# Kernel optimization log

Measured on AMD Instinct MI355X. Metric: run time of the kernel, lower is better.

## Reference

```python
import math
import jax, jax.numpy as jnp
from jax import lax
import numpy as np

D = 256; H = 8; NL = 6; HALF = D // 2
B = 32; NEV = 256

def sinpos(x):
    # SinusoidalPosEmb: (..., ) int -> (..., D)
    freq = jnp.exp(jnp.arange(HALF, dtype=jnp.float32) * (-math.log(10000.0) / (HALF - 1)))
    e = x.astype(jnp.float32)[..., None] * freq
    return jnp.concatenate([jnp.sin(e), jnp.cos(e)], axis=-1)

def layer_norm(x, g, b, eps=1e-5):
    m = x.mean(-1, keepdims=True)
    v = ((x - m) ** 2).mean(-1, keepdims=True)
    return (x - m) / jnp.sqrt(v + eps) * g + b

def gelu(x):
    return jax.nn.gelu(x, approximate=False)

def conv1d(x, w, b, stride):
    y = lax.conv_general_dilated(x, w, (stride,), [(3, 3)], dimension_numbers=("NCH", "OIH", "NCH"))
    return y + b[None, :, None]

def setup_inputs():
    ks = iter(jax.random.split(jax.random.key(0), 48))
    def p(*shape):
        return jax.random.normal(next(ks), shape, dtype=jnp.float32) * 0.02
    inp = dict(
        mel=jax.random.normal(next(ks), (B, 80, 2000), dtype=jnp.float32),
        events=jnp.sort(jax.random.randint(next(ks), (B, NEV), 0, 2000), axis=-1),
        event_mask=jnp.zeros((B, NEV), dtype=bool),
        star_rating=jax.random.uniform(next(ks), (B,), dtype=jnp.float32) * 9.0,
        mel_W=p(16, 80), mel_b=p(16),
        conv1_w=p(128, 16, 7), conv1_b=p(128),
        gn_g=jnp.ones(128, jnp.float32), gn_b=jnp.zeros(128, jnp.float32),
        conv2_w=p(256, 128, 7), conv2_b=p(256),
        cn_g=jnp.ones(D, jnp.float32), cn_b=jnp.zeros(D, jnp.float32),
        star_table=p(20, D),
        ep_W1=p(D, 3 * D), ep_b1=p(D), ep_W2=p(D, D), ep_b2=p(D),
        tl_Wqkv=p(NL, 3 * D, D), tl_bqkv=p(NL, 3 * D),
        tl_Wo=p(NL, D, D), tl_bo=p(NL, D),
        tl_ln1g=jnp.ones((NL, D), jnp.float32), tl_ln1b=jnp.zeros((NL, D), jnp.float32),
        tl_ln2g=jnp.ones((NL, D), jnp.float32), tl_ln2b=jnp.zeros((NL, D), jnp.float32),
        tl_W1=p(NL, 4 * D, D), tl_b1=p(NL, 4 * D),
        tl_W2=p(NL, D, 4 * D), tl_b2=p(NL, D),
        pool_q=jax.random.normal(next(ks), (D,), dtype=jnp.float32),
        on_g=jnp.ones(D, jnp.float32), on_b=jnp.zeros(D, jnp.float32),
        oh_W=p(1, D), oh_b=p(1),
    )
    return inp

def reference(mel, events, event_mask, star_rating, mel_W, mel_b, conv1_w, conv1_b, gn_g, gn_b, conv2_w, conv2_b, cn_g, cn_b, star_table, ep_W1, ep_b1, ep_W2, ep_b2, tl_Wqkv, tl_bqkv, tl_Wo, tl_bo, tl_ln1g, tl_ln1b, tl_ln2g, tl_ln2b, tl_W1, tl_b1, tl_W2, tl_b2, pool_q, on_g, on_b, oh_W, oh_b):
    Bsz = mel.shape[0]
    # mel_compress on channel dim: (B,80,T) -> (B,16,T)
    x_mel = jnp.einsum('bct,oc->bot', mel, mel_W) + mel_b[None, :, None]
    h = gelu(conv1d(x_mel, conv1_w, conv1_b, 2))           # (B,128,1000)
    # GroupNorm(1, C): normalize over (C, L) per sample
    m = h.mean((1, 2), keepdims=True)
    v = ((h - m) ** 2).mean((1, 2), keepdims=True)
    h = (h - m) / jnp.sqrt(v + 1e-5) * gn_g[None, :, None] + gn_b[None, :, None]
    h = gelu(conv1d(h, conv2_w, conv2_b, 2))               # (B,256,500)
    x = h.transpose(0, 2, 1)                               # (B,500,256)
    x = layer_norm(x, cn_g, cn_b)
    S = x.shape[1]
    x = x + sinpos(jnp.arange(S))[None]
    star_bucket = jnp.clip((star_rating / 0.5).astype(jnp.int32), 0, star_table.shape[0] - 1)
    x = x + star_table[star_bucket][:, None, :]
    # --- event gap/ratio embeddings (vectorized; exact match to torch loop when all valid) ---
    diff = jnp.maximum(events[:, 1:] - events[:, :-1], 1)  # clamp(min=1)
    g = jnp.concatenate([diff[:, :1], diff], axis=1)        # g[0] = g[1]
    gap_ms = g * 5
    g_f = jnp.maximum(g.astype(jnp.float32), 1.0)
    r = jnp.clip(g_f[:, 1:] / g_f[:, :-1], 0.1, 10.0)
    ones = jnp.ones((Bsz, 1), dtype=jnp.float32)
    ratio_before = (jnp.concatenate([ones, r], axis=1) * 50).astype(jnp.int32)
    ratio_after = (jnp.concatenate([r, ones], axis=1) * 50).astype(jnp.int32)
    combined = jnp.concatenate([sinpos(ratio_before), sinpos(ratio_after), sinpos(gap_ms)], axis=-1)
    ev = gelu(combined @ ep_W1.T + ep_b1) @ ep_W2.T + ep_b2
    ev = jnp.where(event_mask[..., None], 0.0, ev)
    token_pos = jnp.clip(events // 4, 0, S - 1)
    # batched scatter-add of event embeddings into token stream
    x = x.at[jnp.arange(Bsz)[:, None], token_pos].add(ev)
    hd = D // H
    for i in range(NL):
        xn = layer_norm(x, tl_ln1g[i], tl_ln1b[i])
        qkv = xn @ tl_Wqkv[i].T + tl_bqkv[i]
        q, k, vv = jnp.split(qkv, 3, axis=-1)
        q = q.reshape(Bsz, S, H, hd).transpose(0, 2, 1, 3)
        k = k.reshape(Bsz, S, H, hd).transpose(0, 2, 1, 3)
        vv = vv.reshape(Bsz, S, H, hd).transpose(0, 2, 1, 3)
        a = jax.nn.softmax(jnp.einsum('bhqd,bhkd->bhqk', q, k) / math.sqrt(hd), axis=-1)
        o = jnp.einsum('bhqk,bhkd->bhqd', a, vv).transpose(0, 2, 1, 3).reshape(Bsz, S, D)
        x = x + o @ tl_Wo[i].T + tl_bo[i]
        xn = layer_norm(x, tl_ln2g[i], tl_ln2b[i])
        x = x + gelu(xn @ tl_W1[i].T + tl_b1[i]) @ tl_W2[i].T + tl_b2[i]
    # attention pooling + head
    logits = x @ pool_q / math.sqrt(D)
    w = jax.nn.softmax(logits, axis=-1)
    pooled = jnp.einsum('bs,bsd->bd', w, x)
    return (layer_norm(pooled, on_g, on_b) @ oh_W.T + oh_b).squeeze(-1)
```

## Files before the change

### kernel.cpp

```cpp
#include <hip/hip_runtime.h>
#include <math.h>

namespace {
constexpr int kB = 32;
constexpr int kS = 500;
constexpr int kH = 8;
}
#define LKC (-0.07252236513366287)

typedef __attribute__((ext_vector_type(8))) short s16x8;
typedef __attribute__((ext_vector_type(4))) float f32x4;

__device__ __forceinline__ float gelu_f(float x){
  return 0.5f * x * (1.0f + erff(x * 0.7071067811865476f));
}
__device__ __forceinline__ float b2f(short s){
  union { unsigned u; float f; } x; x.u = ((unsigned)(unsigned short)s) << 16; return x.f;
}
__device__ __forceinline__ short f2b(float f){
  unsigned u = __float_as_uint(f);
  unsigned r = (u + 0x7fffu + ((u >> 16) & 1u)) >> 16;
  return (short)r;
}
__device__ __forceinline__ unsigned cvtpk(float lo, float hi){
  unsigned r;
  asm("v_cvt_pk_bf16_f32 %0, %1, %2" : "=v"(r) : "v"(lo), "v"(hi));
  return r;
}

__global__ __launch_bounds__(256) void f2b_kernel(const float* __restrict__ in,
    short* __restrict__ out, int n){
  int i = blockIdx.x * 256 + threadIdx.x;
  if(i < n) out[i] = f2b(in[i]);
}
__global__ __launch_bounds__(128) void conv1w_pad(const float* __restrict__ w, short* __restrict__ out){
  int n = blockIdx.x, k = threadIdx.x;
  out[n*128 + k] = (k < 112) ? f2b(w[n*112 + k]) : (short)0;
}

template<int OUT, bool DOGELU>
__global__ __launch_bounds__(256) void gemm_mfma(const short* __restrict__ A,
    const short* __restrict__ W, const float* __restrict__ bias,
    void* __restrict__ Cv, int M, int N, int K){
  __shared__ __align__(16) short Al[128*64];
  __shared__ __align__(16) short Wl[128*64];
  const int t = threadIdx.x;
  const int wid = t >> 6, lane = t & 63;
  const int m0 = blockIdx.y * 128, n0 = blockIdx.x * 128;
  const int wr = (wid >> 1) * 64, wc = (wid & 1) * 64;
  const int frow = lane & 15, lg = lane >> 4;
  const int rA = t >> 3;
  const int sA = (t & 7) ^ (rA & 7);
  const short* Aq = A + (size_t)(m0 + rA) * K + sA * 8;
  const short* Wq = W + (size_t)(n0 + rA) * K + sA * 8;
  f32x4 acc[4][4] = {};
  for(int k0 = 0; k0 < K; k0 += 64){
    s16x8 av[4], wv[4];
    #pragma unroll
    for(int j = 0; j < 4; ++j){
      av[j] = *(const s16x8*)(Aq + k0 + (size_t)(32*j)*K);
      wv[j] = *(const s16x8*)(Wq + k0 + (size_t)(32*j)*K);
    }
    __syncthreads();
    #pragma unroll
    for(int j = 0; j < 4; ++j){
      *(s16x8*)&Al[t*8 + j*2048] = av[j];
      *(s16x8*)&Wl[t*8 + j*2048] = wv[j];
    }
    __syncthreads();
    #pragma unroll
    for(int kh = 0; kh < 2; ++kh){
      s16x8 a[4], b[4];
      #pragma unroll
      for(int mi = 0; mi < 4; ++mi){
        int r = wr + mi*16 + frow;
        a[mi] = *(const s16x8*)&Al[r*64 + (((kh*4 + lg) ^ (r & 7)) * 8)];
      }
      #pragma unroll
      for(int ni = 0; ni < 4; ++ni){
        int r = wc + ni*16 + frow;
        b[ni] = *(const s16x8*)&Wl[r*64 + (((kh*4 + lg) ^ (r & 7)) * 8)];
      }
      #pragma unroll
      for(int mi = 0; mi < 4; ++mi)
        #pragma unroll
        for(int ni = 0; ni < 4; ++ni)
          acc[mi][ni] = __builtin_amdgcn_mfma_f32_16x16x32_bf16(a[mi], b[ni], acc[mi][ni], 0, 0, 0);
    }
  }
  #pragma unroll
  for(int mi = 0; mi < 4; ++mi){
    #pragma unroll
    for(int ni = 0; ni < 4; ++ni){
      const int col = n0 + wc + ni*16 + (lane & 15);
      const float bv = bias[col];
      #pragma unroll
      for(int r = 0; r < 4; ++r){
        const int row = m0 + wr + mi*16 + (lane >> 4)*4 + r;
        float v = acc[mi][ni][r] + bv;
        if(DOGELU) v = gelu_f(v);
        if(OUT == 0) ((float*)Cv)[(size_t)row*N + col] = v;
        else if(OUT == 1) ((float*)Cv)[(size_t)row*N + col] += v;
        else ((short*)Cv)[(size_t)row*N + col] = f2b(v);
      }
    }
  }
}

template<bool DOGELU>
__global__ __launch_bounds__(512) void gemm512(const short* __restrict__ A,
    const short* __restrict__ W, const float* __restrict__ bias,
    short* __restrict__ C, int M, int N, int K){
  __shared__ __align__(16) short Al[128*64];
  __shared__ __align__(16) short Wl[256*64];
  const int t = threadIdx.x;
  const int wid = t >> 6, lane = t & 63;
  const int m0 = blockIdx.y * 128, n0 = blockIdx.x * 256;
  const int wm = wid >> 2, wn = wid & 3;
  const int frow = lane & 15, lg = lane >> 4;
  const int rA = t >> 3;
  const int sA = (t & 7) ^ (rA & 7);
  const short* Aq = A + (size_t)(m0 + rA) * K + sA * 8;
  const short* Wq = W + (size_t)(n0 + rA) * K + sA * 8;
  f32x4 acc[4][4] = {};
  for(int k0 = 0; k0 < K; k0 += 64){
    s16x8 av[2], wv[4];
    av[0] = *(const s16x8*)(Aq + k0);
    av[1] = *(const s16x8*)(Aq + k0 + (size_t)64*K);
    #pragma unroll
    for(int j = 0; j < 4; ++j)
      wv[j] = *(const s16x8*)(Wq + k0 + (size_t)(64*j)*K);
    __syncthreads();
    *(s16x8*)&Al[t*8] = av[0];
    *(s16x8*)&Al[t*8 + 4096] = av[1];
    #pragma unroll
    for(int j = 0; j < 4; ++j)
      *(s16x8*)&Wl[t*8 + j*4096] = wv[j];
    __syncthreads();
    #pragma unroll
    for(int kh = 0; kh < 2; ++kh){
      s16x8 a[4], b[4];
      #pragma unroll
      for(int mi = 0; mi < 4; ++mi){
        int r = wm*64 + mi*16 + frow;
        a[mi] = *(const s16x8*)&Al[r*64 + (((kh*4 + lg) ^ (r & 7)) * 8)];
      }
      #pragma unroll
      for(int ni = 0; ni < 4; ++ni){
        int r = wn*64 + ni*16 + frow;
        b[ni] = *(const s16x8*)&Wl[r*64 + (((kh*4 + lg) ^ (r & 7)) * 8)];
      }
      #pragma unroll
      for(int mi = 0; mi < 4; ++mi)
        #pragma unroll
        for(int ni = 0; ni < 4; ++ni)
          acc[mi][ni] = __builtin_amdgcn_mfma_f32_16x16x32_bf16(a[mi], b[ni], acc[mi][ni], 0, 0, 0);
    }
  }
  #pragma unroll
  for(int mi = 0; mi < 4; ++mi){
    #pragma unroll
    for(int ni = 0; ni < 4; ++ni){
      const int col = n0 + wn*64 + ni*16 + (lane & 15);
      const float bv = bias[col];
      #pragma unroll
      for(int r = 0; r < 4; ++r){
        const int row = m0 + wm*64 + mi*16 + (lane >> 4)*4 + r;
        float v = acc[mi][ni][r] + bv;
        if(DOGELU) v = gelu_f(v);
        C[(size_t)row*N + col] = f2b(v);
      }
    }
  }
}

template<bool DOLN>
__global__ __launch_bounds__(512) void gemm_ln(const short* __restrict__ A,
    const short* __restrict__ W, const float* __restrict__ bias,
    float* __restrict__ X, const float* __restrict__ lg_, const float* __restrict__ lb_,
    short* __restrict__ XNB, int M, int K){
  __shared__ __align__(16) short Al[64*64];
  __shared__ __align__(16) short Wl[256*64];
  __shared__ float sbuf[64][4];
  const int t = threadIdx.x;
  const int wid = t >> 6, lane = t & 63;
  const int m0 = blockIdx.y * 64;
  const int wm = wid >> 2, wn = wid & 3;
  const int frow = lane & 15, lg = lane >> 4;
  const int lq = lane & 15;
  const int rA = t >> 3;
  const int sA = (t & 7) ^ (rA & 7);
  const short* Aq = A + (size_t)(m0 + rA) * K + sA * 8;
  const short* Wq = W + (size_t)rA * K + sA * 8;
  f32x4 acc[2][4] = {};
  for(int k0 = 0; k0 < K; k0 += 64){
    s16x8 av = *(const s16x8*)(Aq + k0);
    s16x8 wv[4];
    #pragma unroll
    for(int j = 0; j < 4; ++j)
      wv[j] = *(const s16x8*)(Wq + k0 + (size_t)(64*j)*K);
    __syncthreads();
    *(s16x8*)&Al[t*8] = av;
    #pragma unroll
    for(int j = 0; j < 4; ++j)
      *(s16x8*)&Wl[t*8 + j*4096] = wv[j];
    __syncthreads();
    #pragma unroll
    for(int kh = 0; kh < 2; ++kh){
      s16x8 a[2], b[4];
      #pragma unroll
      for(int mi = 0; mi < 2; ++mi){
        int r = wm*32 + mi*16 + frow;
        a[mi] = *(const s16x8*)&Al[r*64 + (((kh*4 + lg) ^ (r & 7)) * 8)];
      }
      #pragma unroll
      for(int ni = 0; ni < 4; ++ni){
        int r = wn*64 + ni*16 + frow;
        b[ni] = *(const s16x8*)&Wl[r*64 + (((kh*4 + lg) ^ (r & 7)) * 8)];
      }
      #pragma unroll
      for(int mi = 0; mi < 2; ++mi)
        #pragma unroll
        for(int ni = 0; ni < 4; ++ni)
          acc[mi][ni] = __builtin_amdgcn_mfma_f32_16x16x32_bf16(a[mi], b[ni], acc[mi][ni], 0, 0, 0);
    }
  }
  float v[2][4][4];
  #pragma unroll
  for(int mi = 0; mi < 2; ++mi)
    #pragma unroll
    for(int ni = 0; ni < 4; ++ni){
      const int col = wn*64 + ni*16 + lq;
      const float bv = bias[col];
      #pragma unroll
      for(int r = 0; r < 4; ++r){
        const int row = m0 + wm*32 + mi*16 + lg*4 + r;
        v[mi][ni][r] = acc[mi][ni][r] + bv + X[(size_t)row*256 + col];
      }
    }
  __syncthreads();
  float vmean[2][4], vrstd[2][4];
  if(DOLN){
    #pragma unroll
    for(int mi = 0; mi < 2; ++mi)
      #pragma unroll
      for(int r = 0; r < 4; ++r){
        float s = v[mi][0][r] + v[mi][1][r] + v[mi][2][r] + v[mi][3][r];
        s += __shfl_xor(s, 1); s += __shfl_xor(s, 2);
        s += __shfl_xor(s, 4); s += __shfl_xor(s, 8);
        if(lq == 0) sbuf[wm*32 + mi*16 + lg*4 + r][wn] = s;
      }
    __syncthreads();
    #pragma unroll
    for(int mi = 0; mi < 2; ++mi)
      #pragma unroll
      for(int r = 0; r < 4; ++r){
        int rl = wm*32 + mi*16 + lg*4 + r;
        vmean[mi][r] = (sbuf[rl][0] + sbuf[rl][1] + sbuf[rl][2] + sbuf[rl][3]) * (1.f/256.f);
      }
    __syncthreads();
    #pragma unroll
    for(int mi = 0; mi < 2; ++mi)
      #pragma unroll
      for(int r = 0; r < 4; ++r){
        float q = 0.f;
        #pragma unroll
        for(int ni = 0; ni < 4; ++ni){ float d = v[mi][ni][r] - vmean[mi][r]; q += d*d; }
        q += __shfl_xor(q, 1); q += __shfl_xor(q, 2);
        q += __shfl_xor(q, 4); q += __shfl_xor(q, 8);
        if(lq == 0) sbuf[wm*32 + mi*16 + lg*4 + r][wn] = q;
      }
    __syncthreads();
    #pragma unroll
    for(int mi = 0; mi < 2; ++mi)
      #pragma unroll
      for(int r = 0; r < 4; ++r){
        int rl = wm*32 + mi*16 + lg*4 + r;
        float Q = sbuf[rl][0] + sbuf[rl][1] + sbuf[rl][2] + sbuf[rl][3];
        vrstd[mi][r] = 1.f / sqrtf(Q * (1.f/256.f) + 1e-5f);
      }
  }
  #pragma unroll
  for(int mi = 0; mi < 2; ++mi)
    #pragma unroll
    for(int ni = 0; ni < 4; ++ni){
      const int col = wn*64 + ni*16 + lq;
      float gg = 0.f, bb = 0.f;
      if(DOLN){ gg = lg_[col]; bb = lb_[col]; }
      #pragma unroll
      for(int r = 0; r < 4; ++r){
        const int row = m0 + wm*32 + mi*16 + lg*4 + r;
        float val = v[mi][ni][r];
        X[(size_t)row*256 + col] = val;
        if(DOLN)
          XNB[(size_t)row*256 + col] = f2b((val - vmean[mi][r]) * vrstd[mi][r] * gg + bb);
      }
    }
}

__global__ __launch_bounds__(256) void mel_kernel(const float* __restrict__ mel,
    const float* __restrict__ W, const float* __restrict__ bias, float* __restrict__ xm){
  __shared__ float Ws[16][80];
  __shared__ float bs[16];
  const int t = threadIdx.x;
  for(int i = t; i < 16*80; i += 256) Ws[i/80][i%80] = W[i];
  if(t < 16) bs[t] = bias[t];
  __syncthreads();
  int blk = blockIdx.x;
  int b = blk >> 3;
  int tc = (blk & 7) * 256 + t;
  if(tc >= 2000) return;
  float acc[16];
  #pragma unroll
  for(int o = 0; o < 16; ++o) acc[o] = bs[o];
  for(int c = 0; c < 80; ++c){
    float v = mel[((size_t)b*80 + c)*2000 + tc];
    #pragma unroll
    for(int o = 0; o < 16; ++o) acc[o] += v * Ws[o][c];
  }
  #pragma unroll
  for(int o = 0; o < 16; ++o) xm[((size_t)b*16 + o)*2000 + tc] = acc[o];
}

__global__ __launch_bounds__(256) void im2col1b(const float* __restrict__ xm, short* __restrict__ A){
  size_t idx = (size_t)blockIdx.x * 256 + threadIdx.x;
  int col = idx & 127;
  size_t row = idx >> 7;
  int t1 = row % 1000, b = row / 1000;
  float v = 0.f;
  if(col < 112){
    int i = col / 7, k = col % 7;
    int src = 2*t1 + k - 3;
    if(src >= 0 && src < 2000) v = xm[((size_t)b*16 + i)*2000 + src];
  }
  A[idx] = f2b(v);
}

__global__ __launch_bounds__(256) void gn_part(const float* __restrict__ h1, double* __restrict__ part){
  int blk = blockIdx.x;
  const float* p = h1 + (size_t)blk * 16000;
  int t = threadIdx.x;
  double s = 0, q = 0;
  for(int i = t; i < 16000; i += 256){ double v = p[i]; s += v; q += v*v; }
  __shared__ double rs[256], rq[256];
  rs[t] = s; rq[t] = q; __syncthreads();
  for(int s2 = 128; s2 > 0; s2 >>= 1){
    if(t < s2){ rs[t] += rs[t+s2]; rq[t] += rq[t+s2]; }
    __syncthreads();
  }
  if(t == 0){ part[blk*2] = rs[0]; part[blk*2+1] = rq[0]; }
}
__global__ __launch_bounds__(256) void gn_final(const double* __restrict__ part, float* __restrict__ stats){
  int t = threadIdx.x;
  int b = t >> 3;
  double s = part[t*2], q = part[t*2+1];
  s += __shfl_xor(s, 1); q += __shfl_xor(q, 1);
  s += __shfl_xor(s, 2); q += __shfl_xor(q, 2);
  s += __shfl_xor(s, 4); q += __shfl_xor(q, 4);
  if((t & 7) == 0){
    double mean = s / 128000.0;
    double var  = q / 128000.0 - mean*mean;
    stats[b*2]   = (float)mean;
    stats[b*2+1] = (float)(1.0 / sqrt(var + 1e-5));
  }
}

__global__ __launch_bounds__(256) void im2col2b(const float* __restrict__ h1,
    const float* __restrict__ stats, const float* __restrict__ gg,
    const float* __restrict__ gb, short* __restrict__ A){
  size_t idx = (size_t)blockIdx.x * 256 + threadIdx.x;
  int col = idx % 896;
  size_t row = idx / 896;
  int t2 = row % 500, b = row / 500;
  int i = col / 7, k = col % 7;
  int src = 2*t2 + k - 3;
  float v = 0.f;
  if(src >= 0 && src < 1000){
    float raw = h1[((size_t)b*1000 + src)*128 + i];
    v = (raw - stats[b*2]) * stats[b*2+1] * gg[i] + gb[i];
  }
  A[idx] = f2b(v);
}

__global__ __launch_bounds__(256) void postconv(const float* __restrict__ xp,
    const float* __restrict__ cg, const float* __restrict__ cb,
    const float* __restrict__ star, const float* __restrict__ stab,
    float* __restrict__ x){
  int row = blockIdx.x, t = threadIdx.x;
  int s = row % 500, b = row / 500;
  __shared__ float red[256];
  float v = xp[(size_t)row*256 + t];
  red[t] = v; __syncthreads();
  for(int s2 = 128; s2 > 0; s2 >>= 1){ if(t < s2) red[t] += red[t+s2]; __syncthreads(); }
  float mean = red[0] / 256.f; __syncthreads();
  float d = v - mean;
  red[t] = d*d; __syncthreads();
  for(int s2 = 128; s2 > 0; s2 >>= 1){ if(t < s2) red[t] += red[t+s2]; __syncthreads(); }
  float rstd = 1.f / sqrtf(red[0]/256.f + 1e-5f);
  int j = t & 127;
  double f = exp((double)j * LKC);
  double a = (double)s * f;
  float pe = (float)(t < 128 ? sin(a) : cos(a));
  int bucket = (int)(star[b] * 2.0f);
  bucket = bucket < 0 ? 0 : (bucket > 19 ? 19 : bucket);
  x[(size_t)row*256 + t] = d*rstd*cg[t] + cb[t] + pe + stab[bucket*256 + t];
}

__global__ __launch_bounds__(256) void event_feat(const int* __restrict__ events, short* __restrict__ comb){
  int blk = blockIdx.x;
  int e = blk & 255, b = blk >> 8;
  const int* ev = events + b*256;
  int t = threadIdx.x;
  auto gof = [&](int i){ int j = i < 1 ? 1 : i; int d = ev[j] - ev[j-1]; return d < 1 ? 1 : d; };
  int gi = gof(e);
  double rb = 1.0, ra = 1.0;
  if(e != 0){
    rb = (double)gi / (double)gof(e-1);
    rb = rb < 0.1 ? 0.1 : (rb > 10.0 ? 10.0 : rb);
  }
  if(e != 255){
    ra = (double)gof(e+1) / (double)gi;
    ra = ra < 0.1 ? 0.1 : (ra > 10.0 ? 10.0 : ra);
  }
  int rbi = (int)(rb * 50.0);
  int rai = (int)(ra * 50.0);
  int gap = 5 * gi;
  int j = t & 127;
  double f = exp((double)j * LKC);
  double a0 = (double)rbi * f, a1 = (double)rai * f, a2 = (double)gap * f;
  size_t base = (size_t)blk * 768;
  comb[base + t]       = f2b((float)(t < 128 ? sin(a0) : cos(a0)));
  comb[base + 256 + t] = f2b((float)(t < 128 ? sin(a1) : cos(a1)));
  comb[base + 512 + t] = f2b((float)(t < 128 ? sin(a2) : cos(a2)));
}

__global__ __launch_bounds__(256) void ev_scatter(const float* __restrict__ evout,
    const int* __restrict__ events, const unsigned char* __restrict__ mask,
    float* __restrict__ x){
  int blk = blockIdx.x;
  int e = blk & 255, b = blk >> 8;
  if(mask[b*256 + e]) return;
  int tp = events[b*256 + e] >> 2;
  tp = tp < 0 ? 0 : (tp > 499 ? 499 : tp);
  int t = threadIdx.x;
  atomicAdd(&x[((size_t)b*500 + tp)*256 + t], evout[(size_t)blk*256 + t]);
}

__global__ __launch_bounds__(256) void ln_rows(const float* __restrict__ x,
    const float* __restrict__ g, const float* __restrict__ b, short* __restrict__ out){
  int row = blockIdx.x, t = threadIdx.x;
  int wid = t >> 6, lane = t & 63;
  __shared__ float sm[8];
  float v = x[(size_t)row*256 + t];
  float s = v;
  #pragma unroll
  for(int o = 1; o < 64; o <<= 1) s += __shfl_xor(s, o);
  if(lane == 0) sm[wid] = s;
  __syncthreads();
  float mean = (sm[0] + sm[1] + sm[2] + sm[3]) * (1.f/256.f);
  float d = v - mean;
  float q = d*d;
  #pragma unroll
  for(int o = 1; o < 64; o <<= 1) q += __shfl_xor(q, o);
  if(lane == 0) sm[4 + wid] = q;
  __syncthreads();
  float rstd = 1.f / sqrtf((sm[4] + sm[5] + sm[6] + sm[7]) * (1.f/256.f) + 1e-5f);
  out[(size_t)row*256 + t] = f2b(d*rstd*g[t] + b[t]);
}

__global__ __launch_bounds__(512) void attn_mfma(const short* __restrict__ qkv,
    short* __restrict__ o){
  __shared__ __align__(16) short Kl[512*40];
  __shared__ __align__(16) short Vt[32*520];
  __shared__ __align__(16) short Pl[8][640];
  const int i = blockIdx.x;
  const int b = (i & 7)*4 + ((i >> 3) & 3);
  const int h = i >> 5;
  const int t = threadIdx.x;
  const int wid = t >> 6, lane = t & 63;
  const int lq = lane & 15, lg = lane >> 4;
  const short* base = qkv + (size_t)b * kS * 768;
  {
    const int c = t & 3;
    for(int idx = t; idx < 2048; idx += 512){
      int row = idx >> 2;
      s16x8 kv = {0,0,0,0,0,0,0,0};
      unsigned vu0 = 0, vu1 = 0, vu2 = 0, vu3 = 0;
      if(row < kS){
        const short* rp = base + (size_t)row*768 + 256 + h*32 + c*8;
        kv = *(const s16x8*)rp;
        uint4 vv = *(const uint4*)(rp + 256);
        vu0 = vv.x; vu1 = vv.y; vu2 = vv.z; vu3 = vv.w;
      }
      *(s16x8*)&Kl[row*40 + c*8] = kv;
      unsigned b0 = (c & 2) ? vu2 : vu0, b1 = (c & 2) ? vu3 : vu1;
      unsigned b2 = (c & 2) ? vu0 : vu2, b3 = (c & 2) ? vu1 : vu3;
      unsigned r0 = (c & 1) ? b1 : b0, r1 = (c & 1) ? b2 : b1;
      unsigned r2 = (c & 1) ? b3 : b2, r3 = (c & 1) ? b0 : b3;
      #pragma unroll
      for(int j0 = 0; j0 < 8; ++j0){
        unsigned w = (j0 >> 1) == 0 ? r0 : (j0 >> 1) == 1 ? r1 : (j0 >> 1) == 2 ? r2 : r3;
        short val = (short)((j0 & 1) ? (w >> 16) : (w & 0xffff));
        int d = c*8 + ((j0 + 2*c) & 7);
        Vt[d*520 + row] = val;
      }
    }
  }
  __syncthreads();
  const float c2 = 0.17677669529663687f * 1.4426950408889634f;
  short* pw = &Pl[wid][0];
  for(int qi = 0; qi < 4; ++qi){
    const int qt = wid*4 + qi;
    const int q0 = qt*16;
    int qrow = q0 + lq; if(qrow > kS-1) qrow = kS-1;
    s16x8 qf = *(const s16x8*)(base + (size_t)qrow*768 + h*32 + lg*8);
    f32x4 sc[32];
    __builtin_amdgcn_s_setprio(1);
    #pragma unroll
    for(int kt = 0; kt < 32; ++kt){
      s16x8 kf = *(const s16x8*)&Kl[(kt*16 + lq)*40 + lg*8];
      f32x4 z = {0.f,0.f,0.f,0.f};
      sc[kt] = __builtin_amdgcn_mfma_f32_16x16x32_bf16(kf, qf, z, 0, 0, 0);
    }
    __builtin_amdgcn_s_setprio(0);
    if(lg >= 1){ sc[31][0] = -1e30f; sc[31][1] = -1e30f; sc[31][2] = -1e30f; sc[31][3] = -1e30f; }
    float l0 = 0.f, l1 = 0.f, l2 = 0.f, l3 = 0.f;
    #pragma unroll
    for(int kt = 0; kt < 32; ++kt){
      float p0 = exp2f(sc[kt][0] * c2);
      float p1 = exp2f(sc[kt][1] * c2);
      float p2 = exp2f(sc[kt][2] * c2);
      float p3 = exp2f(sc[kt][3] * c2);
      sc[kt][0] = p0; sc[kt][1] = p1; sc[kt][2] = p2; sc[kt][3] = p3;
      l0 += p0; l1 += p1; l2 += p2; l3 += p3;
    }
    float l = (l0 + l1) + (l2 + l3);
    l += __shfl_xor(l, 16, 64);
    l += __shfl_xor(l, 32, 64);
    f32x4 oa0 = {0.f,0.f,0.f,0.f}, oa1 = {0.f,0.f,0.f,0.f};
    #pragma unroll
    for(int kt2 = 0; kt2 < 16; ++kt2){
      f32x4 p0 = sc[kt2*2], p1 = sc[kt2*2+1];
      uint2 pk0, pk1;
      pk0.x = cvtpk(p0[0], p0[1]); pk0.y = cvtpk(p0[2], p0[3]);
      pk1.x = cvtpk(p1[0], p1[1]); pk1.y = cvtpk(p1[2], p1[3]);
      *(uint2*)&pw[lq*40 + lg*4] = pk0;
      *(uint2*)&pw[lq*40 + 16 + lg*4] = pk1;
      s16x8 pf = *(const s16x8*)&pw[lq*40 + lg*8];
      s16x8 v0 = *(const s16x8*)&Vt[lq*520 + kt2*32 + lg*8];
      s16x8 v1 = *(const s16x8*)&Vt[(16+lq)*520 + kt2*32 + lg*8];
      __builtin_amdgcn_s_setprio(1);
      oa0 = __builtin_amdgcn_mfma_f32_16x16x32_bf16(v0, pf, oa0, 0, 0, 0);
      oa1 = __builtin_amdgcn_mfma_f32_16x16x32_bf16(v1, pf, oa1, 0, 0, 0);
      __builtin_amdgcn_s_setprio(0);
    }
    float inv = 1.f / l;
    int qw = q0 + lq;
    if(qw < kS){
      short* op = o + ((size_t)(b*kS + qw))*256 + h*32;
      uint2 w0, w1;
      w0.x = cvtpk(oa0[0]*inv, oa0[1]*inv); w0.y = cvtpk(oa0[2]*inv, oa0[3]*inv);
      w1.x = cvtpk(oa1[0]*inv, oa1[1]*inv); w1.y = cvtpk(oa1[2]*inv, oa1[3]*inv);
      *(uint2*)&op[lg*4] = w0;
      *(uint2*)&op[16 + lg*4] = w1;
    }
  }
}

__global__ __launch_bounds__(256) void pool_head(const float* __restrict__ x,
    const float* __restrict__ pq, const float* __restrict__ og, const float* __restrict__ ob,
    const float* __restrict__ ohW, const float* __restrict__ ohb, float* __restrict__ out){
  int b = blockIdx.x, t = threadIdx.x;
  __shared__ float lg[500];
  __shared__ float red[256];
  const float* xb = x + (size_t)b * 500 * 256;
  for(int s = t; s < 500; s += 256){
    const float* xr = xb + (size_t)s * 256;
    float d = 0.f;
    for(int c = 0; c < 256; ++c) d += xr[c] * pq[c];
    lg[s] = d * 0.0625f;
  }
  __syncthreads();
  float m = -1e30f;
  for(int s = t; s < 500; s += 256) m = fmaxf(m, lg[s]);
  red[t] = m; __syncthreads();
  for(int s2 = 128; s2 > 0; s2 >>= 1){ if(t < s2) red[t] = fmaxf(red[t], red[t+s2]); __syncthreads(); }
  m = red[0]; __syncthreads();
  float ps = 0.f;
  for(int s = t; s < 500; s += 256){ float e = expf(lg[s] - m); lg[s] = e; ps += e; }
  red[t] = ps; __syncthreads();
  for(int s2 = 128; s2 > 0; s2 >>= 1){ if(t < s2) red[t] += red[t+s2]; __syncthreads(); }
  float inv = 1.f / red[0];
  __syncthreads();
  float acc = 0.f;
  for(int s = 0; s < 500; ++s) acc += lg[s] * xb[(size_t)s*256 + t];
  acc *= inv;
  __syncthreads();
  red[t] = acc; __syncthreads();
  for(int s2 = 128; s2 > 0; s2 >>= 1){ if(t < s2) red[t] += red[t+s2]; __syncthreads(); }
  float mean = red[0] / 256.f; __syncthreads();
  float d = acc - mean;
  red[t] = d*d; __syncthreads();
  for(int s2 = 128; s2 > 0; s2 >>= 1){ if(t < s2) red[t] += red[t+s2]; __syncthreads(); }
  float rstd = 1.f / sqrtf(red[0]/256.f + 1e-5f);
  __syncthreads();
  float val = (d*rstd*og[t] + ob[t]) * ohW[t];
  red[t] = val; __syncthreads();
  for(int s2 = 128; s2 > 0; s2 >>= 1){ if(t < s2) red[t] += red[t+s2]; __syncthreads(); }
  if(t == 0) out[b] = red[0] + ohb[0];
}

extern "C" void kernel_launch(void* const* d_in, const int* in_sizes, int n_in,
                              void* d_out, int out_size, void* d_ws, size_t ws_size,
                              hipStream_t stream){
  const float* mel      = (const float*)d_in[0];
  const int*   events   = (const int*)d_in[1];
  const unsigned char* emask = (const unsigned char*)d_in[2];
  const float* star     = (const float*)d_in[3];
  const float* mel_W    = (const float*)d_in[4];
  const float* mel_b    = (const float*)d_in[5];
  const float* conv1_w  = (const float*)d_in[6];
  const float* conv1_b  = (const float*)d_in[7];
  const float* gn_g     = (const float*)d_in[8];
  const float* gn_b     = (const float*)d_in[9];
  const float* conv2_w  = (const float*)d_in[10];
  const float* conv2_b  = (const float*)d_in[11];
  const float* cn_g     = (const float*)d_in[12];
  const float* cn_b     = (const float*)d_in[13];
  const float* star_tab = (const float*)d_in[14];
  const float* ep_W1    = (const float*)d_in[15];
  const float* ep_b1    = (const float*)d_in[16];
  const float* ep_W2    = (const float*)d_in[17];
  const float* ep_b2    = (const float*)d_in[18];
  const float* tl_Wqkv  = (const float*)d_in[19];
  const float* tl_bqkv  = (const float*)d_in[20];
  const float* tl_Wo    = (const float*)d_in[21];
  const float* tl_bo    = (const float*)d_in[22];
  const float* tl_ln1g  = (const float*)d_in[23];
  const float* tl_ln1b  = (const float*)d_in[24];
  const float* tl_ln2g  = (const float*)d_in[25];
  const float* tl_ln2b  = (const float*)d_in[26];
  const float* tl_W1    = (const float*)d_in[27];
  const float* tl_b1    = (const float*)d_in[28];
  const float* tl_W2    = (const float*)d_in[29];
  const float* tl_b2    = (const float*)d_in[30];
  const float* pool_q   = (const float*)d_in[31];
  const float* on_g     = (const float*)d_in[32];
  const float* on_b     = (const float*)d_in[33];
  const float* oh_W     = (const float*)d_in[34];
  const float* oh_b     = (const float*)d_in[35];
  (void)in_sizes; (void)n_in; (void)out_size; (void)ws_size;

  float* ws  = (float*)d_ws;
  float* X   = ws;
  short* XNB = (short*)(ws + 4096000);
  short* OB  = (short*)(ws + 6144000);
  short* WB  = (short*)(ws + 8192000);
  float* BIG = ws + 10812000;
  double* PART = (double*)(ws + 28668000);
  float* STATS = ws + 28671900;

  short* WBc1 = WB + 0;
  short* WBc2 = WB + 16384;
  short* WBe1 = WB + 245760;
  short* WBe2 = WB + 442368;
  short* WBqk = WB + 507904;
  short* WBwo = WB + 1687552;
  short* WBw1 = WB + 2080768;
  short* WBw2 = WB + 3653632;

  float* XMEL = BIG;
  short* A1B  = (short*)(BIG + 1024000);
  float* H1   = BIG + 3072000;
  short* A2B  = (short*)(BIG + 7168000);
  float* XPRE = BIG;
  short* COMBB= (short*)BIG;
  short* EHIDB= (short*)(BIG + 3146000);
  float* EVO  = BIG + 4195000;
  short* QKVB = (short*)BIG;
  short* HIDB = (short*)(BIG + 7168000);

  conv1w_pad<<<128, 128, 0, stream>>>(conv1_w, WBc1);
  f2b_kernel<<<896, 256, 0, stream>>>(conv2_w, WBc2, 229376);
  f2b_kernel<<<768, 256, 0, stream>>>(ep_W1, WBe1, 196608);
  f2b_kernel<<<256, 256, 0, stream>>>(ep_W2, WBe2, 65536);
  f2b_kernel<<<4608, 256, 0, stream>>>(tl_Wqkv, WBqk, 1179648);
  f2b_kernel<<<1536, 256, 0, stream>>>(tl_Wo, WBwo, 393216);
  f2b_kernel<<<6144, 256, 0, stream>>>(tl_W1, WBw1, 1572864);
  f2b_kernel<<<6144, 256, 0, stream>>>(tl_W2, WBw2, 1572864);

  mel_kernel<<<kB*8, 256, 0, stream>>>(mel, mel_W, mel_b, XMEL);
  im2col1b<<<16000, 256, 0, stream>>>(XMEL, A1B);
  gemm_mfma<0,true><<<dim3(1, 250), 256, 0, stream>>>(A1B, WBc1, conv1_b, H1, 32000, 128, 128);
  gn_part<<<256, 256, 0, stream>>>(H1, PART);
  gn_final<<<1, 256, 0, stream>>>(PART, STATS);
  im2col2b<<<56000, 256, 0, stream>>>(H1, STATS, gn_g, gn_b, A2B);
  gemm_mfma<0,true><<<dim3(2, 125), 256, 0, stream>>>(A2B, WBc2, conv2_b, XPRE, 16000, 256, 896);
  postconv<<<16000, 256, 0, stream>>>(XPRE, cn_g, cn_b, star, star_tab, X);
  event_feat<<<kB*256, 256, 0, stream>>>(events, COMBB);
  gemm_mfma<2,true><<<dim3(2, 64), 256, 0, stream>>>(COMBB, WBe1, ep_b1, EHIDB, 8192, 256, 768);
  gemm_mfma<0,false><<<dim3(2, 64), 256, 0, stream>>>(EHIDB, WBe2, ep_b2, EVO, 8192, 256, 256);
  ev_scatter<<<kB*256, 256, 0, stream>>>(EVO, events, emask, X);

  ln_rows<<<16000, 256, 0, stream>>>(X, tl_ln1g, tl_ln1b, XNB);
  for(int i = 0; i < 6; ++i){
    gemm512<false><<<dim3(3, 125), 512, 0, stream>>>(XNB, WBqk + (size_t)i*196608, tl_bqkv + i*768, QKVB, 16000, 768, 256);
    attn_mfma<<<kB*kH, 512, 0, stream>>>(QKVB, OB);
    gemm_ln<true><<<dim3(1, 250), 512, 0, stream>>>(OB, WBwo + (size_t)i*65536, tl_bo + i*256,
        X, tl_ln2g + i*256, tl_ln2b + i*256, XNB, 16000, 256);
    gemm512<true><<<dim3(4, 125), 512, 0, stream>>>(XNB, WBw1 + (size_t)i*262144, tl_b1 + i*1024, HIDB, 16000, 1024, 256);
    if(i < 5)
      gemm_ln<true><<<dim3(1, 250), 512, 0, stream>>>(HIDB, WBw2 + (size_t)i*262144, tl_b2 + i*256,
          X, tl_ln1g + (i+1)*256, tl_ln1b + (i+1)*256, XNB, 16000, 1024);
    else
      gemm_ln<false><<<dim3(1, 250), 512, 0, stream>>>(HIDB, WBw2 + (size_t)i*262144, tl_b2 + i*256,
          X, tl_ln1g, tl_ln1b, XNB, 16000, 1024);
  }

  pool_head<<<kB, 256, 0, stream>>>(X, pool_q, on_g, on_b, oh_W, oh_b, (float*)d_out);
}
```

Measured before the change: 870.8 us.

## Split attention blocks by query half, shuffle P fragments, fuse weight conversions

The attention kernel now launches twice as many blocks, each handling half of the query tiles for a (batch, head) pair. This raises occupancy across the CUs, at the cost of loading K and V into LDS twice. The P-matrix repack through a per-wave LDS scratch is replaced by cross-lane shuffles, which removes the LDS store and load round trip. The seven separate fp32-to-bf16 weight conversion launches are merged into one kernel to cut launch overhead.

```diff
diff --git a/kernel.cpp b/kernel.cpp
--- a/kernel.cpp
+++ b/kernel.cpp
@@ -28,14 +28,26 @@
   return r;
 }
 
-__global__ __launch_bounds__(256) void f2b_kernel(const float* __restrict__ in,
-    short* __restrict__ out, int n){
-  int i = blockIdx.x * 256 + threadIdx.x;
-  if(i < n) out[i] = f2b(in[i]);
-}
 __global__ __launch_bounds__(128) void conv1w_pad(const float* __restrict__ w, short* __restrict__ out){
   int n = blockIdx.x, k = threadIdx.x;
   out[n*128 + k] = (k < 112) ? f2b(w[n*112 + k]) : (short)0;
+}
+
+__global__ __launch_bounds__(256) void f2b_all(const float* __restrict__ c2,
+    const float* __restrict__ e1, const float* __restrict__ e2,
+    const float* __restrict__ qk, const float* __restrict__ wo,
+    const float* __restrict__ w1, const float* __restrict__ w2,
+    short* __restrict__ WB){
+  int blk = blockIdx.x, t = threadIdx.x;
+  const float* src; short* dst; int idx;
+  if(blk < 896){        src = c2; dst = WB + 16384;   idx = blk*256 + t; }
+  else if(blk < 1664){  src = e1; dst = WB + 245760;  idx = (blk-896)*256 + t; }
+  else if(blk < 1920){  src = e2; dst = WB + 442368;  idx = (blk-1664)*256 + t; }
+  else if(blk < 6528){  src = qk; dst = WB + 507904;  idx = (blk-1920)*256 + t; }
+  else if(blk < 8064){  src = wo; dst = WB + 1687552; idx = (blk-6528)*256 + t; }
+  else if(blk < 14208){ src = w1; dst = WB + 2080768; idx = (blk-8064)*256 + t; }
+  else {                src = w2; dst = WB + 3653632; idx = (blk-14208)*256 + t; }
+  dst[idx] = f2b(src[idx]);
 }
 
 template<int OUT, bool DOGELU>
@@ -472,10 +484,10 @@
     short* __restrict__ o){
   __shared__ __align__(16) short Kl[512*40];
   __shared__ __align__(16) short Vt[32*520];
-  __shared__ __align__(16) short Pl[8][640];
   const int i = blockIdx.x;
   const int b = (i & 7)*4 + ((i >> 3) & 3);
-  const int h = i >> 5;
+  const int h = (i >> 5) & 7;
+  const int half = i >> 8;
   const int t = threadIdx.x;
   const int wid = t >> 6, lane = t & 63;
   const int lq = lane & 15, lg = lane >> 4;
@@ -508,9 +520,8 @@
   }
   __syncthreads();
   const float c2 = 0.17677669529663687f * 1.4426950408889634f;
-  short* pw = &Pl[wid][0];
-  for(int qi = 0; qi < 4; ++qi){
-    const int qt = wid*4 + qi;
+  for(int qi = 0; qi < 2; ++qi){
+    const int qt = half*16 + wid*2 + qi;
     const int q0 = qt*16;
     int qrow = q0 + lq; if(qrow > kS-1) qrow = kS-1;
     s16x8 qf = *(const s16x8*)(base + (size_t)qrow*768 + h*32 + lg*8);
@@ -537,16 +548,27 @@
     float l = (l0 + l1) + (l2 + l3);
     l += __shfl_xor(l, 16, 64);
     l += __shfl_xor(l, 32, 64);
+    const int s0l = lq + ((lg & 1) << 5);
+    const int s1l = s0l + 16;
+    const bool fh = (lg & 2) != 0;
     f32x4 oa0 = {0.f,0.f,0.f,0.f}, oa1 = {0.f,0.f,0.f,0.f};
     #pragma unroll
     for(int kt2 = 0; kt2 < 16; ++kt2){
       f32x4 p0 = sc[kt2*2], p1 = sc[kt2*2+1];
-      uint2 pk0, pk1;
-      pk0.x = cvtpk(p0[0], p0[1]); pk0.y = cvtpk(p0[2], p0[3]);
-      pk1.x = cvtpk(p1[0], p1[1]); pk1.y = cvtpk(p1[2], p1[3]);
-      *(uint2*)&pw[lq*40 + lg*4] = pk0;
-      *(uint2*)&pw[lq*40 + 16 + lg*4] = pk1;
-      s16x8 pf = *(const s16x8*)&pw[lq*40 + lg*8];
+      unsigned pk00 = cvtpk(p0[0], p0[1]);
+      unsigned pk01 = cvtpk(p0[2], p0[3]);
+      unsigned pk10 = cvtpk(p1[0], p1[1]);
+      unsigned pk11 = cvtpk(p1[2], p1[3]);
+      unsigned x00 = __shfl(pk00, s0l, 64), x10 = __shfl(pk10, s0l, 64);
+      unsigned x01 = __shfl(pk01, s0l, 64), x11 = __shfl(pk11, s0l, 64);
+      unsigned x02 = __shfl(pk00, s1l, 64), x12 = __shfl(pk10, s1l, 64);
+      unsigned x03 = __shfl(pk01, s1l, 64), x13 = __shfl(pk11, s1l, 64);
+      union { uint4 u; s16x8 s; } pdu;
+      pdu.u.x = fh ? x10 : x00;
+      pdu.u.y = fh ? x11 : x01;
+      pdu.u.z = fh ? x12 : x02;
+      pdu.u.w = fh ? x13 : x03;
+      s16x8 pf = pdu.s;
       s16x8 v0 = *(const s16x8*)&Vt[lq*520 + kt2*32 + lg*8];
       s16x8 v1 = *(const s16x8*)&Vt[(16+lq)*520 + kt2*32 + lg*8];
       __builtin_amdgcn_s_setprio(1);
@@ -661,9 +683,9 @@
   float* STATS = ws + 28671900;
 
   short* WBc1 = WB + 0;
-  short* WBc2 = WB + 16384;
   short* WBe1 = WB + 245760;
   short* WBe2 = WB + 442368;
+  short* WBc2 = WB + 16384;
   short* WBqk = WB + 507904;
   short* WBwo = WB + 1687552;
   short* WBw1 = WB + 2080768;
@@ -681,13 +703,7 @@
   short* HIDB = (short*)(BIG + 7168000);
 
   conv1w_pad<<<128, 128, 0, stream>>>(conv1_w, WBc1);
-  f2b_kernel<<<896, 256, 0, stream>>>(conv2_w, WBc2, 229376);
-  f2b_kernel<<<768, 256, 0, stream>>>(ep_W1, WBe1, 196608);
-  f2b_kernel<<<256, 256, 0, stream>>>(ep_W2, WBe2, 65536);
-  f2b_kernel<<<4608, 256, 0, stream>>>(tl_Wqkv, WBqk, 1179648);
-  f2b_kernel<<<1536, 256, 0, stream>>>(tl_Wo, WBwo, 393216);
-  f2b_kernel<<<6144, 256, 0, stream>>>(tl_W1, WBw1, 1572864);
-  f2b_kernel<<<6144, 256, 0, stream>>>(tl_W2, WBw2, 1572864);
+  f2b_all<<<20352, 256, 0, stream>>>(conv2_w, ep_W1, ep_W2, tl_Wqkv, tl_Wo, tl_W1, tl_W2, WB);
 
   mel_kernel<<<kB*8, 256, 0, stream>>>(mel, mel_W, mel_b, XMEL);
   im2col1b<<<16000, 256, 0, stream>>>(XMEL, A1B);
@@ -705,7 +721,7 @@
   ln_rows<<<16000, 256, 0, stream>>>(X, tl_ln1g, tl_ln1b, XNB);
   for(int i = 0; i < 6; ++i){
     gemm512<false><<<dim3(3, 125), 512, 0, stream>>>(XNB, WBqk + (size_t)i*196608, tl_bqkv + i*768, QKVB, 16000, 768, 256);
-    attn_mfma<<<kB*kH, 512, 0, stream>>>(QKVB, OB);
+    attn_mfma<<<512, 512, 0, stream>>>(QKVB, OB);
     gemm_ln<true><<<dim3(1, 250), 512, 0, stream>>>(OB, WBwo + (size_t)i*65536, tl_bo + i*256,
         X, tl_ln2g + i*256, tl_ln2b + i*256, XNB, 16000, 256);
     gemm512<true><<<dim3(4, 125), 512, 0, stream>>>(XNB, WBw1 + (size_t)i*262144, tl_b1 + i*1024, HIDB, 16000, 1024, 256);
```

Result: slower. 931.5 us (+7.0%).

## Split attention over two key halves with a merge kernel; fuse weight conversions

Applied to the files above, without the earlier changes.

Attention now runs as 512 blocks instead of 256. Each block handles one half of the keys and writes unnormalized bf16 partial outputs along with per-row softmax sums. A new merge kernel adds the two halves and normalizes them, so the 256-CU GPU gets better occupancy at the cost of extra global traffic and an extra launch per layer. The softmax has no running max, so summing the unnormalized partials stays consistent, but it adds a bf16 rounding step before normalization. Separately, the seven weight fp32-to-bf16 conversion launches are fused into one kernel.

```diff
diff --git a/kernel.cpp b/kernel.cpp
--- a/kernel.cpp
+++ b/kernel.cpp
@@ -28,14 +28,26 @@
   return r;
 }
 
-__global__ __launch_bounds__(256) void f2b_kernel(const float* __restrict__ in,
-    short* __restrict__ out, int n){
-  int i = blockIdx.x * 256 + threadIdx.x;
-  if(i < n) out[i] = f2b(in[i]);
-}
 __global__ __launch_bounds__(128) void conv1w_pad(const float* __restrict__ w, short* __restrict__ out){
   int n = blockIdx.x, k = threadIdx.x;
   out[n*128 + k] = (k < 112) ? f2b(w[n*112 + k]) : (short)0;
+}
+
+__global__ __launch_bounds__(256) void f2b_all(const float* __restrict__ c2,
+    const float* __restrict__ e1, const float* __restrict__ e2,
+    const float* __restrict__ qk, const float* __restrict__ wo,
+    const float* __restrict__ w1, const float* __restrict__ w2,
+    short* __restrict__ WB){
+  int blk = blockIdx.x, t = threadIdx.x;
+  const float* src; short* dst; int idx;
+  if(blk < 896){        src = c2; dst = WB + 16384;   idx = blk*256 + t; }
+  else if(blk < 1664){  src = e1; dst = WB + 245760;  idx = (blk-896)*256 + t; }
+  else if(blk < 1920){  src = e2; dst = WB + 442368;  idx = (blk-1664)*256 + t; }
+  else if(blk < 6528){  src = qk; dst = WB + 507904;  idx = (blk-1920)*256 + t; }
+  else if(blk < 8064){  src = wo; dst = WB + 1687552; idx = (blk-6528)*256 + t; }
+  else if(blk < 14208){ src = w1; dst = WB + 2080768; idx = (blk-8064)*256 + t; }
+  else {                src = w2; dst = WB + 3653632; idx = (blk-14208)*256 + t; }
+  dst[idx] = f2b(src[idx]);
 }
 
 template<int OUT, bool DOGELU>
@@ -468,26 +480,32 @@
   out[(size_t)row*256 + t] = f2b(d*rstd*g[t] + b[t]);
 }
 
-__global__ __launch_bounds__(512) void attn_mfma(const short* __restrict__ qkv,
-    short* __restrict__ o){
-  __shared__ __align__(16) short Kl[512*40];
-  __shared__ __align__(16) short Vt[32*520];
+__global__ __launch_bounds__(512) void attn_part(const short* __restrict__ qkv,
+    short* __restrict__ PA0, short* __restrict__ PA1,
+    float* __restrict__ PL0, float* __restrict__ PL1){
+  __shared__ __align__(16) short Kl[256*40];
+  __shared__ __align__(16) short Vt[32*264];
   __shared__ __align__(16) short Pl[8][640];
   const int i = blockIdx.x;
   const int b = (i & 7)*4 + ((i >> 3) & 3);
-  const int h = i >> 5;
+  const int ksp = (i >> 5) & 1;
+  const int h = (i >> 6) & 7;
   const int t = threadIdx.x;
   const int wid = t >> 6, lane = t & 63;
   const int lq = lane & 15, lg = lane >> 4;
   const short* base = qkv + (size_t)b * kS * 768;
+  short* PA = ksp ? PA1 : PA0;
+  float* PL = ksp ? PL1 : PL0;
+  const int k0base = ksp * 256;
   {
     const int c = t & 3;
-    for(int idx = t; idx < 2048; idx += 512){
+    for(int idx = t; idx < 1024; idx += 512){
       int row = idx >> 2;
+      int grow = k0base + row;
       s16x8 kv = {0,0,0,0,0,0,0,0};
       unsigned vu0 = 0, vu1 = 0, vu2 = 0, vu3 = 0;
-      if(row < kS){
-        const short* rp = base + (size_t)row*768 + 256 + h*32 + c*8;
+      if(grow < kS){
+        const short* rp = base + (size_t)grow*768 + 256 + h*32 + c*8;
         kv = *(const s16x8*)rp;
         uint4 vv = *(const uint4*)(rp + 256);
         vu0 = vv.x; vu1 = vv.y; vu2 = vv.z; vu3 = vv.w;
@@ -502,7 +520,7 @@
         unsigned w = (j0 >> 1) == 0 ? r0 : (j0 >> 1) == 1 ? r1 : (j0 >> 1) == 2 ? r2 : r3;
         short val = (short)((j0 & 1) ? (w >> 16) : (w & 0xffff));
         int d = c*8 + ((j0 + 2*c) & 7);
-        Vt[d*520 + row] = val;
+        Vt[d*264 + row] = val;
       }
     }
   }
@@ -514,19 +532,19 @@
     const int q0 = qt*16;
     int qrow = q0 + lq; if(qrow > kS-1) qrow = kS-1;
     s16x8 qf = *(const s16x8*)(base + (size_t)qrow*768 + h*32 + lg*8);
-    f32x4 sc[32];
+    f32x4 sc[16];
     __builtin_amdgcn_s_setprio(1);
     #pragma unroll
-    for(int kt = 0; kt < 32; ++kt){
+    for(int kt = 0; kt < 16; ++kt){
       s16x8 kf = *(const s16x8*)&Kl[(kt*16 + lq)*40 + lg*8];
       f32x4 z = {0.f,0.f,0.f,0.f};
       sc[kt] = __builtin_amdgcn_mfma_f32_16x16x32_bf16(kf, qf, z, 0, 0, 0);
     }
     __builtin_amdgcn_s_setprio(0);
-    if(lg >= 1){ sc[31][0] = -1e30f; sc[31][1] = -1e30f; sc[31][2] = -1e30f; sc[31][3] = -1e30f; }
+    if(ksp == 1 && lg >= 1){ sc[15][0] = -1e30f; sc[15][1] = -1e30f; sc[15][2] = -1e30f; sc[15][3] = -1e30f; }
     float l0 = 0.f, l1 = 0.f, l2 = 0.f, l3 = 0.f;
     #pragma unroll
-    for(int kt = 0; kt < 32; ++kt){
+    for(int kt = 0; kt < 16; ++kt){
       float p0 = exp2f(sc[kt][0] * c2);
       float p1 = exp2f(sc[kt][1] * c2);
       float p2 = exp2f(sc[kt][2] * c2);
@@ -539,7 +557,7 @@
     l += __shfl_xor(l, 32, 64);
     f32x4 oa0 = {0.f,0.f,0.f,0.f}, oa1 = {0.f,0.f,0.f,0.f};
     #pragma unroll
-    for(int kt2 = 0; kt2 < 16; ++kt2){
+    for(int kt2 = 0; kt2 < 8; ++kt2){
       f32x4 p0 = sc[kt2*2], p1 = sc[kt2*2+1];
       uint2 pk0, pk1;
       pk0.x = cvtpk(p0[0], p0[1]); pk0.y = cvtpk(p0[2], p0[3]);
@@ -547,24 +565,47 @@
       *(uint2*)&pw[lq*40 + lg*4] = pk0;
       *(uint2*)&pw[lq*40 + 16 + lg*4] = pk1;
       s16x8 pf = *(const s16x8*)&pw[lq*40 + lg*8];
-      s16x8 v0 = *(const s16x8*)&Vt[lq*520 + kt2*32 + lg*8];
-      s16x8 v1 = *(const s16x8*)&Vt[(16+lq)*520 + kt2*32 + lg*8];
+      s16x8 v0 = *(const s16x8*)&Vt[lq*264 + kt2*32 + lg*8];
+      s16x8 v1 = *(const s16x8*)&Vt[(16+lq)*264 + kt2*32 + lg*8];
       __builtin_amdgcn_s_setprio(1);
       oa0 = __builtin_amdgcn_mfma_f32_16x16x32_bf16(v0, pf, oa0, 0, 0, 0);
       oa1 = __builtin_amdgcn_mfma_f32_16x16x32_bf16(v1, pf, oa1, 0, 0, 0);
       __builtin_amdgcn_s_setprio(0);
     }
-    float inv = 1.f / l;
     int qw = q0 + lq;
     if(qw < kS){
-      short* op = o + ((size_t)(b*kS + qw))*256 + h*32;
+      short* op = PA + ((size_t)(b*kS + qw))*256 + h*32;
       uint2 w0, w1;
-      w0.x = cvtpk(oa0[0]*inv, oa0[1]*inv); w0.y = cvtpk(oa0[2]*inv, oa0[3]*inv);
-      w1.x = cvtpk(oa1[0]*inv, oa1[1]*inv); w1.y = cvtpk(oa1[2]*inv, oa1[3]*inv);
+      w0.x = cvtpk(oa0[0], oa0[1]); w0.y = cvtpk(oa0[2], oa0[3]);
+      w1.x = cvtpk(oa1[0], oa1[1]); w1.y = cvtpk(oa1[2], oa1[3]);
       *(uint2*)&op[lg*4] = w0;
       *(uint2*)&op[16 + lg*4] = w1;
-    }
-  }
+      if(lg == 0) PL[((size_t)(b*kH + h))*kS + qw] = l;
+    }
+  }
+}
+
+__global__ __launch_bounds__(256) void attn_merge(const short* __restrict__ PA0,
+    const short* __restrict__ PA1, const float* __restrict__ PL0,
+    const float* __restrict__ PL1, short* __restrict__ o){
+  int id = blockIdx.x*256 + threadIdx.x;
+  int e4 = id*4;
+  int row = e4 >> 8;
+  int col = e4 & 255;
+  int h = col >> 5;
+  int b = row / 500, s = row - b*500;
+  size_t g = ((size_t)(b*kH + h))*kS + s;
+  float linv = 1.f / (PL0[g] + PL1[g]);
+  uint2 a0 = *(const uint2*)(PA0 + (size_t)row*256 + col);
+  uint2 a1 = *(const uint2*)(PA1 + (size_t)row*256 + col);
+  uint2 w;
+  float v0 = (b2f((short)(a0.x & 0xffff)) + b2f((short)(a1.x & 0xffff))) * linv;
+  float v1 = (b2f((short)(a0.x >> 16))    + b2f((short)(a1.x >> 16)))    * linv;
+  float v2 = (b2f((short)(a0.y & 0xffff)) + b2f((short)(a1.y & 0xffff))) * linv;
+  float v3 = (b2f((short)(a0.y >> 16))    + b2f((short)(a1.y >> 16)))    * linv;
+  w.x = cvtpk(v0, v1);
+  w.y = cvtpk(v2, v3);
+  *(uint2*)(o + (size_t)row*256 + col) = w;
 }
 
 __global__ __launch_bounds__(256) void pool_head(const float* __restrict__ x,
@@ -678,16 +719,14 @@
   short* EHIDB= (short*)(BIG + 3146000);
   float* EVO  = BIG + 4195000;
   short* QKVB = (short*)BIG;
+  short* PA0  = (short*)(BIG + 6144000);
+  short* PA1  = (short*)(BIG + 8192000);
+  float* PL0  = BIG + 10240000;
+  float* PL1  = BIG + 10368000;
   short* HIDB = (short*)(BIG + 7168000);
 
   conv1w_pad<<<128, 128, 0, stream>>>(conv1_w, WBc1);
-  f2b_kernel<<<896, 256, 0, stream>>>(conv2_w, WBc2, 229376);
-  f2b_kernel<<<768, 256, 0, stream>>>(ep_W1, WBe1, 196608);
-  f2b_kernel<<<256, 256, 0, stream>>>(ep_W2, WBe2, 65536);
-  f2b_kernel<<<4608, 256, 0, stream>>>(tl_Wqkv, WBqk, 1179648);
-  f2b_kernel<<<1536, 256, 0, stream>>>(tl_Wo, WBwo, 393216);
-  f2b_kernel<<<6144, 256, 0, stream>>>(tl_W1, WBw1, 1572864);
-  f2b_kernel<<<6144, 256, 0, stream>>>(tl_W2, WBw2, 1572864);
+  f2b_all<<<20352, 256, 0, stream>>>(conv2_w, ep_W1, ep_W2, tl_Wqkv, tl_Wo, tl_W1, tl_W2, WB);
 
   mel_kernel<<<kB*8, 256, 0, stream>>>(mel, mel_W, mel_b, XMEL);
   im2col1b<<<16000, 256, 0, stream>>>(XMEL, A1B);
@@ -705,7 +744,8 @@
   ln_rows<<<16000, 256, 0, stream>>>(X, tl_ln1g, tl_ln1b, XNB);
   for(int i = 0; i < 6; ++i){
     gemm512<false><<<dim3(3, 125), 512, 0, stream>>>(XNB, WBqk + (size_t)i*196608, tl_bqkv + i*768, QKVB, 16000, 768, 256);
-    attn_mfma<<<kB*kH, 512, 0, stream>>>(QKVB, OB);
+    attn_part<<<512, 512, 0, stream>>>(QKVB, PA0, PA1, PL0, PL1);
+    attn_merge<<<4000, 256, 0, stream>>>(PA0, PA1, PL0, PL1, OB);
     gemm_ln<true><<<dim3(1, 250), 512, 0, stream>>>(OB, WBwo + (size_t)i*65536, tl_bo + i*256,
         X, tl_ln2g + i*256, tl_ln2b + i*256, XNB, 16000, 256);
     gemm512<true><<<dim3(4, 125), 512, 0, stream>>>(XNB, WBw1 + (size_t)i*262144, tl_b1 + i*1024, HIDB, 16000, 1024, 256);
```

Measured after the change: 885.8 us. Within noise of the previous version (+1.7%).
